# Optimization experiments

Measured on AMD Instinct MI355X. Metric: run time of the kernel, lower is better.

## Reference

```python
import jax, jax.numpy as jnp
import numpy as np

GRAPH_WEIGHT = 0.3


def setup_inputs() -> dict:
    key = jax.random.key(0)
    ks = jax.random.split(key, 6)
    B, N, NB, MAXKV, BS = 8, 1048576, 8192, 32, 128
    logits = jax.random.normal(ks[0], (B, N, 1), dtype=jnp.float32)
    targets = jax.random.bernoulli(ks[1], 0.5, (B, N)).astype(jnp.float32)
    sup_mask = jax.random.bernoulli(ks[2], 0.1, (B, N))
    ignore_mask = jax.random.bernoulli(ks[3], 0.05, (B, N))
    kv_indices = jax.random.randint(ks[4], (B, NB, MAXKV), 0, NB)
    kv_num_blocks = jax.random.randint(ks[5], (B, NB), 0, MAXKV + 1)
    return {
        "logits": logits,
        "targets": targets,
        "sup_mask": sup_mask,
        "ignore_mask": ignore_mask,
        "kv_indices": kv_indices,
        "kv_num_blocks": kv_num_blocks,
        "block_size": BS,
    }


def _loss(logits, targets, sup_mask, ignore_mask, kv_indices, kv_num_blocks, block_size):
    x = logits.squeeze(-1)                      # [B, N]
    B, N = x.shape
    nb = N // block_size
    dt = x.dtype

    # ---- supervised BCE over sup_mask (== BCEWithLogitsLoss on gathered set) ----
    per = jnp.maximum(x, 0) - x * targets + jnp.log1p(jnp.exp(-jnp.abs(x)))
    supf = sup_mask.astype(dt)
    sup_cnt = supf.sum()
    loss_sup = jnp.where(sup_cnt > 0, (per * supf).sum() / jnp.maximum(sup_cnt, 1), jnp.asarray(0, dt))

    # ---- graph smoothness (block-sparse neighbor-mean squared error) ----
    probs = jax.nn.sigmoid(x)                   # [B, N]
    uncertain = (~ignore_mask) & (~sup_mask)
    keep = (~ignore_mask).astype(dt)

    pblk = probs.reshape(B, nb, block_size)     # [B, nb, BS]
    kblk = keep.reshape(B, nb, block_size)
    block_sum = (pblk * kblk).sum(-1)           # [B, nb] sum of non-ignored probs per block
    block_cnt = kblk.sum(-1)                    # [B, nb]

    max_kv = kv_indices.shape[-1]
    flat_idx = kv_indices.reshape(B, nb * max_kv)
    g_sum = jnp.take_along_axis(block_sum, flat_idx, axis=1).reshape(B, nb, max_kv)
    g_cnt = jnp.take_along_axis(block_cnt, flat_idx, axis=1).reshape(B, nb, max_kv)
    kv_valid = (jnp.arange(max_kv)[None, None, :] < kv_num_blocks[..., None]).astype(dt)
    neigh_sum = (g_sum * kv_valid).sum(-1)      # [B, nb]
    neigh_cnt = (g_cnt * kv_valid).sum(-1)
    neigh_mean = neigh_sum / jnp.maximum(neigh_cnt, 1)

    ublk = uncertain.reshape(B, nb, block_size).astype(dt)
    q_cnt = ublk.sum(-1)                        # [B, nb] uncertain q nodes per block
    valid_block = (q_cnt > 0) & (kv_num_blocks > 0) & (neigh_cnt > 0)

    sq = (((pblk - neigh_mean[..., None]) ** 2) * ublk).sum(-1)  # [B, nb]
    vb = valid_block.astype(dt)
    loss_b = (sq * vb).sum(-1)                  # [B]
    count_b = (q_cnt * vb).sum(-1)              # [B]
    batch_valid = count_b > 0
    per_batch = jnp.where(batch_valid, loss_b / jnp.maximum(count_b, 1), 0.0)
    loss_graph = per_batch.sum() / jnp.maximum(batch_valid.sum(), 1).astype(dt)
    loss_graph = jnp.where(uncertain.any(), loss_graph, jnp.asarray(0, dt))

    return loss_sup + GRAPH_WEIGHT * loss_graph


def reference(logits, targets, sup_mask, ignore_mask, kv_indices, kv_num_blocks, block_size):
    return _loss(logits, targets, sup_mask, ignore_mask, kv_indices, kv_num_blocks, block_size)
```

## Files before the change

### kernel.cpp

```cpp
#include <hip/hip_runtime.h>

constexpr int BATCH = 8;
constexpr int NPB   = 1 << 20;
constexpr int BS    = 128;
constexpr int NB    = NPB / BS;
constexpr int NBLK  = BATCH * NB;
constexpr int MAXKV = 32;

#define GRAPH_WEIGHT 0.3f

constexpr int WS_SUP   = 0;
constexpr int WS_GRAPH = 512;
constexpr int WS_ZERO  = 2048;
constexpr int WS_BSUM  = 2048;
constexpr int WS_BCNT  = WS_BSUM + NBLK;
constexpr int WS_QCNT  = WS_BCNT + NBLK;
constexpr int WS_UP    = WS_QCNT + NBLK;
constexpr int WS_UP2   = WS_UP  + NBLK;

__global__ __launch_bounds__(256) void k_phase1(const float* __restrict__ lg,
                                                const float* __restrict__ tg,
                                                const int* __restrict__ sm,
                                                const int* __restrict__ im,
                                                float* __restrict__ ws)
{
    const int tid = blockIdx.x * 256 + threadIdx.x;
    const int e0  = tid << 2;

    const float4 x4 = *reinterpret_cast<const float4*>(lg + e0);
    const float4 t4 = *reinterpret_cast<const float4*>(tg + e0);
    const int4   s4 = *reinterpret_cast<const int4*>(sm + e0);
    const int4   g4 = *reinterpret_cast<const int4*>(im + e0);

    const float xs[4] = {x4.x, x4.y, x4.z, x4.w};
    const float ts[4] = {t4.x, t4.y, t4.z, t4.w};
    const int   ssv[4] = {s4.x, s4.y, s4.z, s4.w};
    const int   ggv[4] = {g4.x, g4.y, g4.z, g4.w};

    float sup_sum = 0.f, sup_cnt = 0.f, u_cnt = 0.f;
    float bsum = 0.f, bcnt = 0.f, q = 0.f, up = 0.f, up2 = 0.f;

#pragma unroll
    for (int j = 0; j < 4; ++j) {
        const float x = xs[j], t = ts[j];
        const bool s = (ssv[j] != 0);
        const bool g = (ggv[j] != 0);

        const float ax  = fabsf(x);
        const float e   = __expf(-ax);
        const float lp  = __logf(1.f + e);
        const float per = fmaxf(x, 0.f) - x * t + lp;
        const float inv = 1.f / (1.f + e);
        const float p   = (x >= 0.f) ? inv : e * inv;

        if (s) { sup_sum += per; sup_cnt += 1.f; }
        if (!g) { bsum += p; bcnt += 1.f; }
        if (!g && !s) { q += 1.f; up += p; up2 += p * p; u_cnt += 1.f; }
    }

#pragma unroll
    for (int d = 16; d >= 1; d >>= 1) {
        bsum += __shfl_xor(bsum, d);
        bcnt += __shfl_xor(bcnt, d);
        q    += __shfl_xor(q, d);
        up   += __shfl_xor(up, d);
        up2  += __shfl_xor(up2, d);
    }
    const int lane = threadIdx.x & 63;
    if ((lane & 31) == 0) {
        const int blk = ((tid >> 6) << 1) + (lane >> 5);
        ws[WS_BSUM + blk] = bsum;
        ws[WS_BCNT + blk] = bcnt;
        ws[WS_QCNT + blk] = q;
        ws[WS_UP   + blk] = up;
        ws[WS_UP2  + blk] = up2;
    }

#pragma unroll
    for (int d = 32; d >= 1; d >>= 1) {
        sup_sum += __shfl_xor(sup_sum, d);
        sup_cnt += __shfl_xor(sup_cnt, d);
        u_cnt   += __shfl_xor(u_cnt, d);
    }
    __shared__ float lds[4][3];
    const int w = threadIdx.x >> 6;
    if (lane == 0) { lds[w][0] = sup_sum; lds[w][1] = sup_cnt; lds[w][2] = u_cnt; }
    __syncthreads();
    if (threadIdx.x == 0) {
        const float a = lds[0][0] + lds[1][0] + lds[2][0] + lds[3][0];
        const float b = lds[0][1] + lds[1][1] + lds[2][1] + lds[3][1];
        const float c = lds[0][2] + lds[1][2] + lds[2][2] + lds[3][2];
        float* slot = ws + WS_SUP + (int)(blockIdx.x & 63) * 8;
        atomicAdd(slot + 0, a);
        atomicAdd(slot + 1, b);
        atomicAdd(slot + 2, c);
    }
}

__global__ __launch_bounds__(256) void k_phase2(const int* __restrict__ kvi,
                                                const int* __restrict__ kvn,
                                                float* __restrict__ ws)
{
    const int tid    = blockIdx.x * 256 + threadIdx.x;
    const int h      = tid >> 5;
    const int lane32 = threadIdx.x & 31;
    const int b      = h >> 13;

    const int nkv = kvn[h];
    const int idx = kvi[(size_t)h * MAXKV + lane32];

    const float* bsum_a = ws + WS_BSUM;
    const float* bcnt_a = ws + WS_BCNT;

    float gs = 0.f, gc = 0.f;
    if (lane32 < nkv) {
        const int src = (h & ~(NB - 1)) + idx;
        gs = bsum_a[src];
        gc = bcnt_a[src];
    }
#pragma unroll
    for (int d = 16; d >= 1; d >>= 1) {
        gs += __shfl_xor(gs, d);
        gc += __shfl_xor(gc, d);
    }

    __shared__ float lds[8][2];
    if (lane32 == 0) {
        const float q   = ws[WS_QCNT + h];
        const float up  = ws[WS_UP   + h];
        const float up2 = ws[WS_UP2  + h];
        const float m   = gs / fmaxf(gc, 1.f);
        const bool  vb  = (q > 0.f) && (nkv > 0) && (gc > 0.f);
        const float sq  = up2 - 2.f * m * up + m * m * q;
        const int hw = threadIdx.x >> 5;
        lds[hw][0] = vb ? sq : 0.f;
        lds[hw][1] = vb ? q  : 0.f;
    }
    __syncthreads();
    if (threadIdx.x == 0) {
        float L = 0.f, C = 0.f;
#pragma unroll
        for (int j = 0; j < 8; ++j) { L += lds[j][0]; C += lds[j][1]; }
        float* slot = ws + WS_GRAPH + b * 128 + (int)(blockIdx.x & 15) * 8;
        atomicAdd(slot + 0, L);
        atomicAdd(slot + 1, C);
    }
}

__global__ __launch_bounds__(64) void k_phase3(const float* __restrict__ ws,
                                               float* __restrict__ out)
{
    const int lane = threadIdx.x;

    float ss = ws[WS_SUP + lane * 8 + 0];
    float sc = ws[WS_SUP + lane * 8 + 1];
    float uc = ws[WS_SUP + lane * 8 + 2];
#pragma unroll
    for (int d = 32; d >= 1; d >>= 1) {
        ss += __shfl_xor(ss, d);
        sc += __shfl_xor(sc, d);
        uc += __shfl_xor(uc, d);
    }

    float per_sum = 0.f, nvalid = 0.f;
    for (int b = 0; b < BATCH; ++b) {
        float l = 0.f, c = 0.f;
        if (lane < 16) {
            l = ws[WS_GRAPH + b * 128 + lane * 8 + 0];
            c = ws[WS_GRAPH + b * 128 + lane * 8 + 1];
        }
#pragma unroll
        for (int d = 32; d >= 1; d >>= 1) {
            l += __shfl_xor(l, d);
            c += __shfl_xor(c, d);
        }
        if (c > 0.f) { per_sum += l / fmaxf(c, 1.f); nvalid += 1.f; }
    }

    if (lane == 0) {
        const float loss_sup = (sc > 0.f) ? ss / fmaxf(sc, 1.f) : 0.f;
        float lg = per_sum / fmaxf(nvalid, 1.f);
        if (!(uc > 0.f)) lg = 0.f;
        out[0] = loss_sup + GRAPH_WEIGHT * lg;
    }
}

extern "C" void kernel_launch(void* const* d_in, const int* in_sizes, int n_in,
                              void* d_out, int out_size, void* d_ws, size_t ws_size,
                              hipStream_t stream) {
    const float* lg  = (const float*)d_in[0];
    const float* tg  = (const float*)d_in[1];
    const int*   sm  = (const int*)d_in[2];
    const int*   im  = (const int*)d_in[3];
    const int*   kvi = (const int*)d_in[4];
    const int*   kvn = (const int*)d_in[5];
    float* ws  = (float*)d_ws;
    float* out = (float*)d_out;

    hipMemsetAsync(d_ws, 0, WS_ZERO * sizeof(float), stream);

    k_phase1<<<(BATCH * NPB) / (4 * 256), 256, 0, stream>>>(lg, tg, sm, im, ws);
    k_phase2<<<(NBLK * 32) / 256, 256, 0, stream>>>(kvi, kvn, ws);
    k_phase3<<<1, 64, 0, stream>>>(ws, out);
}
```

Baseline: 190.0 us.

## Process 16 elements per thread and pack per-block stats into vector records

Phase 1 now has each thread handle four float4 chunks, so the grid shrinks fourfold. An 8-lane group owns each 128-element block, which cuts the block reduction to three shuffle steps. Per-block statistics are stored as packed float2 (sum, count) and float4 (q, up, up2) records, so phase 2 needs one vectorized load instead of several scalar gathers. The uncertain count now travels through the per-batch graph slots in phase 2 rather than as a third atomic in phase 1. The cost is fewer resident waves for hiding memory latency and higher register use per thread.

```diff
diff --git a/kernel.cpp b/kernel.cpp
--- a/kernel.cpp
+++ b/kernel.cpp
@@ -12,88 +12,85 @@
 constexpr int WS_SUP   = 0;
 constexpr int WS_GRAPH = 512;
 constexpr int WS_ZERO  = 2048;
-constexpr int WS_BSUM  = 2048;
-constexpr int WS_BCNT  = WS_BSUM + NBLK;
-constexpr int WS_QCNT  = WS_BCNT + NBLK;
-constexpr int WS_UP    = WS_QCNT + NBLK;
-constexpr int WS_UP2   = WS_UP  + NBLK;
-
-__global__ __launch_bounds__(256) void k_phase1(const float* __restrict__ lg,
-                                                const float* __restrict__ tg,
-                                                const int* __restrict__ sm,
-                                                const int* __restrict__ im,
+constexpr int WS_BSC   = 2048;
+constexpr int WS_QUP   = WS_BSC + 2 * NBLK;
+
+__global__ __launch_bounds__(256) void k_phase1(const float4* __restrict__ lg4,
+                                                const float4* __restrict__ tg4,
+                                                const int4* __restrict__ sm4,
+                                                const int4* __restrict__ im4,
                                                 float* __restrict__ ws)
 {
-    const int tid = blockIdx.x * 256 + threadIdx.x;
-    const int e0  = tid << 2;
-
-    const float4 x4 = *reinterpret_cast<const float4*>(lg + e0);
-    const float4 t4 = *reinterpret_cast<const float4*>(tg + e0);
-    const int4   s4 = *reinterpret_cast<const int4*>(sm + e0);
-    const int4   g4 = *reinterpret_cast<const int4*>(im + e0);
-
-    const float xs[4] = {x4.x, x4.y, x4.z, x4.w};
-    const float ts[4] = {t4.x, t4.y, t4.z, t4.w};
-    const int   ssv[4] = {s4.x, s4.y, s4.z, s4.w};
-    const int   ggv[4] = {g4.x, g4.y, g4.z, g4.w};
-
-    float sup_sum = 0.f, sup_cnt = 0.f, u_cnt = 0.f;
+    const int lane = threadIdx.x & 63;
+    const int wid  = (blockIdx.x << 2) + (threadIdx.x >> 6);
+    const int grp  = lane >> 3;
+    const int sub  = lane & 7;
+    const int blk  = (wid << 3) + grp;
+    const int c0   = (blk << 5) + sub;
+
+    float sup_sum = 0.f, sup_cnt = 0.f;
     float bsum = 0.f, bcnt = 0.f, q = 0.f, up = 0.f, up2 = 0.f;
 
 #pragma unroll
     for (int j = 0; j < 4; ++j) {
-        const float x = xs[j], t = ts[j];
-        const bool s = (ssv[j] != 0);
-        const bool g = (ggv[j] != 0);
-
-        const float ax  = fabsf(x);
-        const float e   = __expf(-ax);
-        const float lp  = __logf(1.f + e);
-        const float per = fmaxf(x, 0.f) - x * t + lp;
-        const float inv = 1.f / (1.f + e);
-        const float p   = (x >= 0.f) ? inv : e * inv;
-
-        if (s) { sup_sum += per; sup_cnt += 1.f; }
-        if (!g) { bsum += p; bcnt += 1.f; }
-        if (!g && !s) { q += 1.f; up += p; up2 += p * p; u_cnt += 1.f; }
-    }
-
-#pragma unroll
-    for (int d = 16; d >= 1; d >>= 1) {
+        const int c = c0 + (j << 3);
+        const float4 x4 = lg4[c];
+        const float4 t4 = tg4[c];
+        const int4   s4 = sm4[c];
+        const int4   g4 = im4[c];
+
+        const float xs[4]  = {x4.x, x4.y, x4.z, x4.w};
+        const float ts[4]  = {t4.x, t4.y, t4.z, t4.w};
+        const int   ssv[4] = {s4.x, s4.y, s4.z, s4.w};
+        const int   ggv[4] = {g4.x, g4.y, g4.z, g4.w};
+
+#pragma unroll
+        for (int k = 0; k < 4; ++k) {
+            const float x = xs[k], t = ts[k];
+            const bool s = (ssv[k] != 0);
+            const bool g = (ggv[k] != 0);
+
+            const float ax  = fabsf(x);
+            const float e   = __expf(-ax);
+            const float lp  = __logf(1.f + e);
+            const float per = fmaxf(x, 0.f) - x * t + lp;
+            const float inv = 1.f / (1.f + e);
+            const float p   = (x >= 0.f) ? inv : e * inv;
+
+            if (s) { sup_sum += per; sup_cnt += 1.f; }
+            if (!g) { bsum += p; bcnt += 1.f; }
+            if (!g && !s) { q += 1.f; up += p; up2 += p * p; }
+        }
+    }
+
+#pragma unroll
+    for (int d = 4; d >= 1; d >>= 1) {
         bsum += __shfl_xor(bsum, d);
         bcnt += __shfl_xor(bcnt, d);
         q    += __shfl_xor(q, d);
         up   += __shfl_xor(up, d);
         up2  += __shfl_xor(up2, d);
     }
-    const int lane = threadIdx.x & 63;
-    if ((lane & 31) == 0) {
-        const int blk = ((tid >> 6) << 1) + (lane >> 5);
-        ws[WS_BSUM + blk] = bsum;
-        ws[WS_BCNT + blk] = bcnt;
-        ws[WS_QCNT + blk] = q;
-        ws[WS_UP   + blk] = up;
-        ws[WS_UP2  + blk] = up2;
+    if (sub == 0) {
+        *reinterpret_cast<float2*>(ws + WS_BSC + 2 * blk) = make_float2(bsum, bcnt);
+        *reinterpret_cast<float4*>(ws + WS_QUP + 4 * blk) = make_float4(q, up, up2, 0.f);
     }
 
 #pragma unroll
     for (int d = 32; d >= 1; d >>= 1) {
         sup_sum += __shfl_xor(sup_sum, d);
         sup_cnt += __shfl_xor(sup_cnt, d);
-        u_cnt   += __shfl_xor(u_cnt, d);
-    }
-    __shared__ float lds[4][3];
+    }
+    __shared__ float lds[4][2];
     const int w = threadIdx.x >> 6;
-    if (lane == 0) { lds[w][0] = sup_sum; lds[w][1] = sup_cnt; lds[w][2] = u_cnt; }
+    if (lane == 0) { lds[w][0] = sup_sum; lds[w][1] = sup_cnt; }
     __syncthreads();
     if (threadIdx.x == 0) {
         const float a = lds[0][0] + lds[1][0] + lds[2][0] + lds[3][0];
         const float b = lds[0][1] + lds[1][1] + lds[2][1] + lds[3][1];
-        const float c = lds[0][2] + lds[1][2] + lds[2][2] + lds[3][2];
         float* slot = ws + WS_SUP + (int)(blockIdx.x & 63) * 8;
         atomicAdd(slot + 0, a);
         atomicAdd(slot + 1, b);
-        atomicAdd(slot + 2, c);
     }
 }
 
@@ -109,14 +106,11 @@
     const int nkv = kvn[h];
     const int idx = kvi[(size_t)h * MAXKV + lane32];
 
-    const float* bsum_a = ws + WS_BSUM;
-    const float* bcnt_a = ws + WS_BCNT;
-
     float gs = 0.f, gc = 0.f;
     if (lane32 < nkv) {
         const int src = (h & ~(NB - 1)) + idx;
-        gs = bsum_a[src];
-        gc = bcnt_a[src];
+        const float2 v = *reinterpret_cast<const float2*>(ws + WS_BSC + 2 * src);
+        gs = v.x; gc = v.y;
     }
 #pragma unroll
     for (int d = 16; d >= 1; d >>= 1) {
@@ -124,26 +118,27 @@
         gc += __shfl_xor(gc, d);
     }
 
-    __shared__ float lds[8][2];
+    __shared__ float lds[8][3];
     if (lane32 == 0) {
-        const float q   = ws[WS_QCNT + h];
-        const float up  = ws[WS_UP   + h];
-        const float up2 = ws[WS_UP2  + h];
-        const float m   = gs / fmaxf(gc, 1.f);
-        const bool  vb  = (q > 0.f) && (nkv > 0) && (gc > 0.f);
-        const float sq  = up2 - 2.f * m * up + m * m * q;
+        const float4 quv = *reinterpret_cast<const float4*>(ws + WS_QUP + 4 * h);
+        const float q = quv.x, up = quv.y, up2 = quv.z;
+        const float m  = gs / fmaxf(gc, 1.f);
+        const bool  vb = (q > 0.f) && (nkv > 0) && (gc > 0.f);
+        const float sq = up2 - 2.f * m * up + m * m * q;
         const int hw = threadIdx.x >> 5;
         lds[hw][0] = vb ? sq : 0.f;
         lds[hw][1] = vb ? q  : 0.f;
+        lds[hw][2] = q;
     }
     __syncthreads();
     if (threadIdx.x == 0) {
-        float L = 0.f, C = 0.f;
-#pragma unroll
-        for (int j = 0; j < 8; ++j) { L += lds[j][0]; C += lds[j][1]; }
+        float L = 0.f, C = 0.f, U = 0.f;
+#pragma unroll
+        for (int j = 0; j < 8; ++j) { L += lds[j][0]; C += lds[j][1]; U += lds[j][2]; }
         float* slot = ws + WS_GRAPH + b * 128 + (int)(blockIdx.x & 15) * 8;
         atomicAdd(slot + 0, L);
         atomicAdd(slot + 1, C);
+        atomicAdd(slot + 2, U);
     }
 }
 
@@ -154,27 +149,28 @@
 
     float ss = ws[WS_SUP + lane * 8 + 0];
     float sc = ws[WS_SUP + lane * 8 + 1];
-    float uc = ws[WS_SUP + lane * 8 + 2];
 #pragma unroll
     for (int d = 32; d >= 1; d >>= 1) {
         ss += __shfl_xor(ss, d);
         sc += __shfl_xor(sc, d);
-        uc += __shfl_xor(uc, d);
-    }
-
-    float per_sum = 0.f, nvalid = 0.f;
+    }
+
+    float per_sum = 0.f, nvalid = 0.f, uc = 0.f;
     for (int b = 0; b < BATCH; ++b) {
-        float l = 0.f, c = 0.f;
+        float l = 0.f, c = 0.f, u = 0.f;
         if (lane < 16) {
             l = ws[WS_GRAPH + b * 128 + lane * 8 + 0];
             c = ws[WS_GRAPH + b * 128 + lane * 8 + 1];
+            u = ws[WS_GRAPH + b * 128 + lane * 8 + 2];
         }
 #pragma unroll
         for (int d = 32; d >= 1; d >>= 1) {
             l += __shfl_xor(l, d);
             c += __shfl_xor(c, d);
+            u += __shfl_xor(u, d);
         }
         if (c > 0.f) { per_sum += l / fmaxf(c, 1.f); nvalid += 1.f; }
+        uc += u;
     }
 
     if (lane == 0) {
@@ -188,18 +184,18 @@
 extern "C" void kernel_launch(void* const* d_in, const int* in_sizes, int n_in,
                               void* d_out, int out_size, void* d_ws, size_t ws_size,
                               hipStream_t stream) {
-    const float* lg  = (const float*)d_in[0];
-    const float* tg  = (const float*)d_in[1];
-    const int*   sm  = (const int*)d_in[2];
-    const int*   im  = (const int*)d_in[3];
-    const int*   kvi = (const int*)d_in[4];
-    const int*   kvn = (const int*)d_in[5];
+    const float4* lg4 = (const float4*)d_in[0];
+    const float4* tg4 = (const float4*)d_in[1];
+    const int4*   sm4 = (const int4*)d_in[2];
+    const int4*   im4 = (const int4*)d_in[3];
+    const int*    kvi = (const int*)d_in[4];
+    const int*    kvn = (const int*)d_in[5];
     float* ws  = (float*)d_ws;
     float* out = (float*)d_out;
 
     hipMemsetAsync(d_ws, 0, WS_ZERO * sizeof(float), stream);
 
-    k_phase1<<<(BATCH * NPB) / (4 * 256), 256, 0, stream>>>(lg, tg, sm, im, ws);
+    k_phase1<<<(BATCH * NPB) / (16 * 256), 256, 0, stream>>>(lg4, tg4, sm4, im4, ws);
     k_phase2<<<(NBLK * 32) / 256, 256, 0, stream>>>(kvi, kvn, ws);
     k_phase3<<<1, 64, 0, stream>>>(ws, out);
 }
```

After: 201.3 us. 6.0% more time.
